# Kernel optimization log

Measured on AMD Instinct MI355X. Metric: run time of the kernel, lower is better.

The kernel has to match this reference:

```python
import jax, jax.numpy as jnp
import numpy as np

N_NODES = 100000
N_EDGES = 1600000
IN_FEATS = 64
N_CLASSES = 64


def setup_inputs() -> dict:
    key = jax.random.key(0)
    k1, k2, k3, k4, k5 = jax.random.split(key, 5)
    feat = jax.random.normal(k1, (N_NODES, IN_FEATS), dtype=jnp.float32)
    edge_row = jnp.sort(jax.random.randint(k2, (N_EDGES,), 0, N_NODES))
    edge_col = jax.random.randint(k3, (N_EDGES,), 0, N_NODES)
    # values of the cached normalized adjacency power (all positive, ~1/deg scale)
    edge_val = jax.random.uniform(k4, (N_EDGES,), dtype=jnp.float32) / 16.0
    # nn.Linear(in_feats, n_classes): weight [C, F] (xavier), bias zeros
    limit = float(np.sqrt(6.0 / (IN_FEATS + N_CLASSES)))
    W = jax.random.uniform(k5, (N_CLASSES, IN_FEATS), dtype=jnp.float32,
                           minval=-limit, maxval=limit)
    b = jnp.zeros((N_CLASSES,), dtype=jnp.float32)
    return {"feat": feat, "edge_row": edge_row, "edge_col": edge_col,
            "edge_val": edge_val, "W": W, "b": b}


def reference(feat, edge_row, edge_col, edge_val, W, b):
    # SpMM: h = A_pre @ feat, A_pre given as COO (edge_row, edge_col, edge_val)
    msg = edge_val[:, None] * feat[edge_col]          # [E, F] gather + scale
    h = jax.ops.segment_sum(msg, edge_row, num_segments=N_NODES)  # [N, F]
    # fc: Linear(in_feats -> n_classes), norm=None so no normalization
    return h @ W.T + b                                 # [N, C]
```

## Files before the change

kernel.cpp:

```cpp
#include <hip/hip_runtime.h>
#include <hip/hip_bf16.h>

typedef __attribute__((ext_vector_type(8))) short short8;
typedef __attribute__((ext_vector_type(4))) float f32x4;

__device__ __forceinline__ unsigned short f2bf(float x) {
    unsigned int u = __float_as_uint(x);
    unsigned int lsb = (u >> 16) & 1u;
    u += 0x7fffu + lsb;
    return (unsigned short)(u >> 16);
}

__device__ __forceinline__ short8 pack8(f32x4 a, f32x4 b) {
    short8 r;
    r[0] = (short)f2bf(a.x); r[1] = (short)f2bf(a.y);
    r[2] = (short)f2bf(a.z); r[3] = (short)f2bf(a.w);
    r[4] = (short)f2bf(b.x); r[5] = (short)f2bf(b.y);
    r[6] = (short)f2bf(b.z); r[7] = (short)f2bf(b.w);
    return r;
}

__global__ __launch_bounds__(256) void k_init(const float* __restrict__ bias,
                                              float* __restrict__ out, long total4) {
    long i4 = (long)blockIdx.x * 256 + threadIdx.x;
    if (i4 < total4) {
        const f32x4* b4 = (const f32x4*)bias;
        ((f32x4*)out)[i4] = b4[i4 & 15];
    }
}

__global__ __launch_bounds__(256) void k_setup(const float* __restrict__ feat,
                                               const float* __restrict__ W,
                                               const float* __restrict__ bias,
                                               unsigned short* __restrict__ G,
                                               float* __restrict__ out,
                                               int N, int gblocks) {
    if ((int)blockIdx.x >= gblocks) {
        long i4 = (long)(blockIdx.x - gblocks) * 256 + threadIdx.x;
        long total4 = (long)N * 16;
        if (i4 < total4) {
            const f32x4* b4 = (const f32x4*)bias;
            ((f32x4*)out)[i4] = b4[i4 & 15];
        }
        return;
    }

    int wave = blockIdx.x * 4 + (threadIdx.x >> 6);
    int lane = threadIdx.x & 63;
    int m0 = wave * 16;
    if (m0 >= N) return;
    int n = lane & 15;
    int quad = lane >> 4;

    short8 bf[4][2];
#pragma unroll
    for (int ct = 0; ct < 4; ++ct)
#pragma unroll
        for (int ks = 0; ks < 2; ++ks) {
            const f32x4* wp = (const f32x4*)(W + (size_t)(ct * 16 + n) * 64 + ks * 32 + quad * 8);
            f32x4 w0 = wp[0];
            f32x4 w1 = wp[1];
            bf[ct][ks] = pack8(w0, w1);
        }

    int mrow = m0 + n; if (mrow >= N) mrow = N - 1;
    short8 af[2];
#pragma unroll
    for (int ks = 0; ks < 2; ++ks) {
        const f32x4* ap = (const f32x4*)(feat + (size_t)mrow * 64 + ks * 32 + quad * 8);
        f32x4 a0 = __builtin_nontemporal_load(ap);
        f32x4 a1 = __builtin_nontemporal_load(ap + 1);
        af[ks] = pack8(a0, a1);
    }

    f32x4 acc[4];
#pragma unroll
    for (int ct = 0; ct < 4; ++ct) {
        acc[ct] = (f32x4){0.f, 0.f, 0.f, 0.f};
#pragma unroll
        for (int ks = 0; ks < 2; ++ks)
            acc[ct] = __builtin_amdgcn_mfma_f32_16x16x32_bf16(af[ks], bf[ct][ks], acc[ct], 0, 0, 0);
    }

#pragma unroll
    for (int ct = 0; ct < 4; ++ct)
#pragma unroll
        for (int r = 0; r < 4; ++r) {
            int rowm = m0 + quad * 4 + r;
            if (rowm < N)
                G[(size_t)rowm * 64 + ct * 16 + n] = f2bf(acc[ct][r]);
        }
}

__global__ __launch_bounds__(256) void k_spmm(const unsigned short* __restrict__ G,
                                              const int* __restrict__ erow,
                                              const int* __restrict__ ecol,
                                              const float* __restrict__ evalv,
                                              const float* __restrict__ bias,
                                              float* __restrict__ out, int E) {
    int b = blockIdx.x;
    int fg  = (b & 7) >> 2;
    int sub = (b >> 3) * 4 + (b & 3);
    int wavein = threadIdx.x >> 6;
    int lane = threadIdx.x & 63;
    long base0 = ((long)sub * 4 + wavein) * 256;
    if (base0 >= E) return;

    int q  = lane >> 4;
    int fs = lane & 15;
    int vq4 = q << 2;
    unsigned voff = (unsigned)fs * 4u;
    const char* Gb = (const char*)G + ((unsigned)fg << 6);
    float2 b2 = ((const float2*)bias)[fg * 16 + fs];

    float acc0 = 0.f, acc1 = 0.f;
    bool first = true;
    int cur;

    auto flush_atomic = [&]() {
        float t0 = acc0 + __shfl_xor(acc0, 16);
        float t1 = acc1 + __shfl_xor(acc1, 16);
        t0 += __shfl_xor(t0, 32);
        t1 += __shfl_xor(t1, 32);
        if (lane < 16) {
            float* p = out + ((size_t)(unsigned)cur << 6) + (unsigned)(fg * 32 + fs * 2);
            atomicAdd(p, t0);
            atomicAdd(p + 1, t1);
        }
        acc0 = 0.f; acc1 = 0.f;
    };
    auto flush = [&]() {
        if (first) { flush_atomic(); first = false; return; }
        float t0 = acc0 + __shfl_xor(acc0, 16);
        float t1 = acc1 + __shfl_xor(acc1, 16);
        t0 += __shfl_xor(t0, 32);
        t1 += __shfl_xor(t1, 32);
        if (lane < 16) {
            float* p = out + ((size_t)(unsigned)cur << 6) + (unsigned)(fg * 32 + fs * 2);
            float2 o; o.x = b2.x + t0; o.y = b2.y + t1;
            *(float2*)p = o;
        }
        acc0 = 0.f; acc1 = 0.f;
    };

    if (base0 + 256 <= E) {
        long i0 = base0 + lane;
        int rv[4], cv[4], vvv[4];
#pragma unroll
        for (int c = 0; c < 4; ++c) {
            rv[c]  = __builtin_nontemporal_load(erow + i0 + 64 * c);
            cv[c]  = __builtin_nontemporal_load(ecol + i0 + 64 * c);
            vvv[c] = __builtin_nontemporal_load((const int*)evalv + i0 + 64 * c);
        }
        cur = __builtin_amdgcn_readlane(rv[0], 0);

        unsigned long long bm[4];
#pragma unroll
        for (int c = 0; c < 4; ++c) {
            int rn = __shfl_down(rv[c], 1);
            unsigned long long m = __ballot(rv[c] != rn) & 0x7fffffffffffffffULL;
            int r63 = __builtin_amdgcn_readlane(rv[c], 63);
            int n0  = (c < 3) ? __builtin_amdgcn_readlane(rv[c + 1], 0) : (r63 + 1);
            if (r63 != n0) m |= 0x8000000000000000ULL;
            bm[c] = m;
        }

        unsigned gbuf[3][8];

#define SPMM_ISSUE(GI, SLOT) do {                                              \
    _Pragma("unroll")                                                          \
    for (int k_ = 0; k_ < 8; ++k_) {                                           \
        const int p_  = (GI) * 8 + k_;                   \
        const int c_  = p_ >> 4;                                    \
        const int pj_ = p_ & 15;                        \
        int idx_ = vq4 + 16 * pj_;                                             \
        int colv_ = __builtin_amdgcn_ds_bpermute(idx_, cv[c_]);                \
        unsigned off_ = ((unsigned)colv_ << 7) + voff;                         \
        gbuf[SLOT][k_] = *(const unsigned*)(Gb + off_);                        \
    } } while (0)

        SPMM_ISSUE(0, 0);
        SPMM_ISSUE(1, 1);

#pragma unroll
        for (int g = 0; g < 8; ++g) {
            if (g < 6) SPMM_ISSUE(g + 2, (g + 2) % 3);
            __builtin_amdgcn_sched_barrier(0);

#pragma unroll
            for (int k = 0; k < 8; ++k) {
                const int p  = g * 8 + k;
                const int c  = p >> 4;
                const int pj = p & 15;
                const int i4 = pj * 4;
                int idx = vq4 + i4 * 4;
                float vs = __int_as_float(__builtin_amdgcn_ds_bpermute(idx, vvv[c]));
                unsigned u = gbuf[g % 3][k];
                float flo = __uint_as_float(u << 16);
                float fhi = __uint_as_float(u & 0xffff0000u);
                bool slow = (pj == 0) ? ((c > 0 && ((bm[c - 1] >> 63) & 1ULL)) || (bm[c] & 7ULL) != 0)
                                      : (((bm[c] >> (4 * pj - 1)) & 0xFULL) != 0);
                if (!slow) {
                    acc0 = fmaf(vs, flo, acc0);
                    acc1 = fmaf(vs, fhi, acc1);
                } else {
                    int r0 = __builtin_amdgcn_readlane(rv[c], i4);
                    int r3 = __builtin_amdgcn_readlane(rv[c], i4 + 3);
                    if (r0 == r3) {
                        if (r0 != cur) { flush(); cur = r0; }
                        acc0 = fmaf(vs, flo, acc0);
                        acc1 = fmaf(vs, fhi, acc1);
                    } else {
                        int rowsv = __builtin_amdgcn_ds_bpermute(idx, rv[c]);
                        int r1 = __builtin_amdgcn_readlane(rv[c], i4 + 1);
                        int r2 = __builtin_amdgcn_readlane(rv[c], i4 + 2);
                        int rr = r0;
                        while (true) {
                            if (rr != cur) { flush(); cur = rr; }
                            float vm = (rowsv == rr) ? vs : 0.f;
                            acc0 = fmaf(vm, flo, acc0);
                            acc1 = fmaf(vm, fhi, acc1);
                            if (rr == r3) break;
                            rr = (r1 > rr) ? r1 : ((r2 > rr) ? r2 : r3);
                        }
                    }
                }
            }
        }
#undef SPMM_ISSUE
    } else {
        cur = erow[base0];
        for (long e = base0; e < (long)E; ++e) {
            int r = erow[e];
            int c = ecol[e];
            float v = evalv[e];
            unsigned u = *(const unsigned*)(Gb + (((unsigned)c << 7) + voff));
            float flo = __uint_as_float(u << 16);
            float fhi = __uint_as_float(u & 0xffff0000u);
            if (r != cur) { flush(); cur = r; }
            float vm = (q == 0) ? v : 0.f;
            acc0 = fmaf(vm, flo, acc0);
            acc1 = fmaf(vm, fhi, acc1);
        }
    }

    flush_atomic();
}

__global__ __launch_bounds__(256) void k_fused(const float* __restrict__ feat,
                                               const int* __restrict__ erow,
                                               const int* __restrict__ ecol,
                                               const float* __restrict__ evalv,
                                               const float* __restrict__ W,
                                               float* __restrict__ out,
                                               int E, int epw) {
    __shared__ float Wt[64 * 64];
    for (int i = threadIdx.x; i < 4096; i += 256) {
        int c = i >> 6, f = i & 63;
        Wt[f * 64 + c] = W[i];
    }
    __syncthreads();

    int wave = blockIdx.x * 4 + (threadIdx.x >> 6);
    int lane = threadIdx.x & 63;
    long e0 = (long)wave * epw;
    if (e0 >= E) return;
    long e1 = e0 + epw; if (e1 > E) e1 = E;

    int cur = erow[e0];
    float acc = 0.f;
    for (long e = e0; e < e1; ++e) {
        int r = erow[e];
        int c = ecol[e];
        float v = evalv[e];
        float g = feat[((size_t)c << 6) | lane];
        if (r != cur) {
            float res = 0.f;
#pragma unroll
            for (int f = 0; f < 64; ++f)
                res += __shfl(acc, f, 64) * Wt[f * 64 + lane];
            atomicAdd(out + ((size_t)cur << 6) + lane, res);
            acc = 0.f;
            cur = r;
        }
        acc += v * g;
    }
    {
        float res = 0.f;
#pragma unroll
        for (int f = 0; f < 64; ++f)
            res += __shfl(acc, f, 64) * Wt[f * 64 + lane];
        atomicAdd(out + ((size_t)cur << 6) + lane, res);
    }
}

extern "C" void kernel_launch(void* const* d_in, const int* in_sizes, int n_in,
                              void* d_out, int out_size, void* d_ws, size_t ws_size,
                              hipStream_t stream) {
    const float* feat  = (const float*)d_in[0];
    const int*   erow  = (const int*)d_in[1];
    const int*   ecol  = (const int*)d_in[2];
    const float* evalv = (const float*)d_in[3];
    const float* W     = (const float*)d_in[4];
    const float* bias  = (const float*)d_in[5];
    float* out = (float*)d_out;

    int N = in_sizes[0] / 64;
    int E = in_sizes[1];

    size_t need = (size_t)N * 64 * sizeof(unsigned short);
    if (ws_size >= need) {
        unsigned short* G = (unsigned short*)d_ws;
        int tiles = (N + 15) / 16;
        int gblocks = (tiles + 3) / 4;
        long total4 = (long)N * 16;
        int iblocks = (int)((total4 + 255) / 256);
        k_setup<<<gblocks + iblocks, 256, 0, stream>>>(feat, W, bias, G, out, N, gblocks);

        int nwpf = (E + 255) / 256;
        int bpf  = (nwpf + 3) / 4;
        int noct = (bpf + 3) / 4;
        k_spmm<<<noct * 8, 256, 0, stream>>>(G, erow, ecol, evalv, bias, out, E);
    } else {
        long total4 = (long)N * 16;
        k_init<<<(int)((total4 + 255) / 256), 256, 0, stream>>>(bias, out, total4);
        int epw = (E + 8191) / 8192;
        if (epw < 32) epw = 32;
        int nwaves = (E + epw - 1) / epw;
        int nblocks = (nwaves + 3) / 4;
        k_fused<<<nblocks, 256, 0, stream>>>(feat, erow, ecol, evalv, W, out, E, epw);
    }
}
```

Before: 164.8 us.

## Quantize projected features to int8 with per-row scales and drop feature-half split

The setup kernel now stores the projected feature matrix as int8 with one float scale per row instead of bf16. The SpMM kernel folds each row's scale into the edge value, and each lane now handles four features instead of two, so one wave covers all 64 features. This removes the two-way feature-group split and halves the bytes gathered per edge. The cost is an extra scattered scale load per edge, heavier dequantization arithmetic, and a notable loss of accuracy from int8 quantization that may break tolerance.

```diff
diff --git a/kernel.cpp b/kernel.cpp
--- a/kernel.cpp
+++ b/kernel.cpp
@@ -32,7 +32,8 @@
 __global__ __launch_bounds__(256) void k_setup(const float* __restrict__ feat,
                                                const float* __restrict__ W,
                                                const float* __restrict__ bias,
-                                               unsigned short* __restrict__ G,
+                                               unsigned char* __restrict__ G8,
+                                               float* __restrict__ scales,
                                                float* __restrict__ out,
                                                int N, int gblocks) {
     if ((int)blockIdx.x >= gblocks) {
@@ -83,64 +84,79 @@
     }
 
 #pragma unroll
-    for (int ct = 0; ct < 4; ++ct)
-#pragma unroll
-        for (int r = 0; r < 4; ++r) {
-            int rowm = m0 + quad * 4 + r;
-            if (rowm < N)
-                G[(size_t)rowm * 64 + ct * 16 + n] = f2bf(acc[ct][r]);
-        }
-}
-
-__global__ __launch_bounds__(256) void k_spmm(const unsigned short* __restrict__ G,
+    for (int r = 0; r < 4; ++r) {
+        float rm = fmaxf(fmaxf(fabsf(acc[0][r]), fabsf(acc[1][r])),
+                         fmaxf(fabsf(acc[2][r]), fabsf(acc[3][r])));
+        rm = fmaxf(rm, __shfl_xor(rm, 1, 16));
+        rm = fmaxf(rm, __shfl_xor(rm, 2, 16));
+        rm = fmaxf(rm, __shfl_xor(rm, 4, 16));
+        rm = fmaxf(rm, __shfl_xor(rm, 8, 16));
+        int rowm = m0 + quad * 4 + r;
+        if (rowm < N) {
+            float inv = (rm > 0.f) ? (127.f / rm) : 0.f;
+            if (n == 0) scales[rowm] = rm * (1.f / 127.f);
+#pragma unroll
+            for (int ct = 0; ct < 4; ++ct) {
+                float qf = rintf(acc[ct][r] * inv);
+                qf = fminf(127.f, fmaxf(-127.f, qf));
+                G8[(size_t)rowm * 64 + ct * 16 + n] = (unsigned char)(signed char)(int)qf;
+            }
+        }
+    }
+}
+
+__global__ __launch_bounds__(256) void k_spmm(const unsigned char* __restrict__ G8,
+                                              const float* __restrict__ scales,
                                               const int* __restrict__ erow,
                                               const int* __restrict__ ecol,
                                               const float* __restrict__ evalv,
                                               const float* __restrict__ bias,
                                               float* __restrict__ out, int E) {
-    int b = blockIdx.x;
-    int fg  = (b & 7) >> 2;
-    int sub = (b >> 3) * 4 + (b & 3);
-    int wavein = threadIdx.x >> 6;
+    int wave = blockIdx.x * 4 + (threadIdx.x >> 6);
     int lane = threadIdx.x & 63;
-    long base0 = ((long)sub * 4 + wavein) * 256;
+    long base0 = (long)wave * 256;
     if (base0 >= E) return;
 
     int q  = lane >> 4;
     int fs = lane & 15;
     int vq4 = q << 2;
     unsigned voff = (unsigned)fs * 4u;
-    const char* Gb = (const char*)G + ((unsigned)fg << 6);
-    float2 b2 = ((const float2*)bias)[fg * 16 + fs];
-
-    float acc0 = 0.f, acc1 = 0.f;
+    f32x4 b4 = ((const f32x4*)bias)[fs];
+
+    float acc0 = 0.f, acc1 = 0.f, acc2 = 0.f, acc3 = 0.f;
     bool first = true;
     int cur;
 
     auto flush_atomic = [&]() {
         float t0 = acc0 + __shfl_xor(acc0, 16);
         float t1 = acc1 + __shfl_xor(acc1, 16);
-        t0 += __shfl_xor(t0, 32);
-        t1 += __shfl_xor(t1, 32);
+        float t2 = acc2 + __shfl_xor(acc2, 16);
+        float t3 = acc3 + __shfl_xor(acc3, 16);
+        t0 += __shfl_xor(t0, 32); t1 += __shfl_xor(t1, 32);
+        t2 += __shfl_xor(t2, 32); t3 += __shfl_xor(t3, 32);
         if (lane < 16) {
-            float* p = out + ((size_t)(unsigned)cur << 6) + (unsigned)(fg * 32 + fs * 2);
-            atomicAdd(p, t0);
+            float* p = out + ((size_t)(unsigned)cur << 6) + ((unsigned)fs << 2);
+            atomicAdd(p + 0, t0);
             atomicAdd(p + 1, t1);
-        }
-        acc0 = 0.f; acc1 = 0.f;
+            atomicAdd(p + 2, t2);
+            atomicAdd(p + 3, t3);
+        }
+        acc0 = acc1 = acc2 = acc3 = 0.f;
     };
     auto flush = [&]() {
         if (first) { flush_atomic(); first = false; return; }
         float t0 = acc0 + __shfl_xor(acc0, 16);
         float t1 = acc1 + __shfl_xor(acc1, 16);
-        t0 += __shfl_xor(t0, 32);
-        t1 += __shfl_xor(t1, 32);
+        float t2 = acc2 + __shfl_xor(acc2, 16);
+        float t3 = acc3 + __shfl_xor(acc3, 16);
+        t0 += __shfl_xor(t0, 32); t1 += __shfl_xor(t1, 32);
+        t2 += __shfl_xor(t2, 32); t3 += __shfl_xor(t3, 32);
         if (lane < 16) {
-            float* p = out + ((size_t)(unsigned)cur << 6) + (unsigned)(fg * 32 + fs * 2);
-            float2 o; o.x = b2.x + t0; o.y = b2.y + t1;
-            *(float2*)p = o;
-        }
-        acc0 = 0.f; acc1 = 0.f;
+            float* p = out + ((size_t)(unsigned)cur << 6) + ((unsigned)fs << 2);
+            f32x4 o = {b4.x + t0, b4.y + t1, b4.z + t2, b4.w + t3};
+            *(f32x4*)p = o;
+        }
+        acc0 = acc1 = acc2 = acc3 = 0.f;
     };
 
     if (base0 + 256 <= E) {
@@ -151,6 +167,8 @@
             rv[c]  = __builtin_nontemporal_load(erow + i0 + 64 * c);
             cv[c]  = __builtin_nontemporal_load(ecol + i0 + 64 * c);
             vvv[c] = __builtin_nontemporal_load((const int*)evalv + i0 + 64 * c);
+            float sc = scales[(unsigned)cv[c]];
+            vvv[c] = __float_as_int(__int_as_float(vvv[c]) * sc);
         }
         cur = __builtin_amdgcn_readlane(rv[0], 0);
 
@@ -175,8 +193,8 @@
         const int pj_ = p_ & 15;                        \
         int idx_ = vq4 + 16 * pj_;                                             \
         int colv_ = __builtin_amdgcn_ds_bpermute(idx_, cv[c_]);                \
-        unsigned off_ = ((unsigned)colv_ << 7) + voff;                         \
-        gbuf[SLOT][k_] = *(const unsigned*)(Gb + off_);                        \
+        unsigned off_ = ((unsigned)colv_ << 6) + voff;                         \
+        gbuf[SLOT][k_] = *(const unsigned*)(G8 + off_);                        \
     } } while (0)
 
         SPMM_ISSUE(0, 0);
@@ -196,20 +214,26 @@
                 int idx = vq4 + i4 * 4;
                 float vs = __int_as_float(__builtin_amdgcn_ds_bpermute(idx, vvv[c]));
                 unsigned u = gbuf[g % 3][k];
-                float flo = __uint_as_float(u << 16);
-                float fhi = __uint_as_float(u & 0xffff0000u);
+                float f0 = (float)((int)(u << 24) >> 24);
+                float f1 = (float)((int)(u << 16) >> 24);
+                float f2 = (float)((int)(u << 8) >> 24);
+                float f3 = (float)((int)u >> 24);
                 bool slow = (pj == 0) ? ((c > 0 && ((bm[c - 1] >> 63) & 1ULL)) || (bm[c] & 7ULL) != 0)
                                       : (((bm[c] >> (4 * pj - 1)) & 0xFULL) != 0);
                 if (!slow) {
-                    acc0 = fmaf(vs, flo, acc0);
-                    acc1 = fmaf(vs, fhi, acc1);
+                    acc0 = fmaf(vs, f0, acc0);
+                    acc1 = fmaf(vs, f1, acc1);
+                    acc2 = fmaf(vs, f2, acc2);
+                    acc3 = fmaf(vs, f3, acc3);
                 } else {
                     int r0 = __builtin_amdgcn_readlane(rv[c], i4);
                     int r3 = __builtin_amdgcn_readlane(rv[c], i4 + 3);
                     if (r0 == r3) {
                         if (r0 != cur) { flush(); cur = r0; }
-                        acc0 = fmaf(vs, flo, acc0);
-                        acc1 = fmaf(vs, fhi, acc1);
+                        acc0 = fmaf(vs, f0, acc0);
+                        acc1 = fmaf(vs, f1, acc1);
+                        acc2 = fmaf(vs, f2, acc2);
+                        acc3 = fmaf(vs, f3, acc3);
                     } else {
                         int rowsv = __builtin_amdgcn_ds_bpermute(idx, rv[c]);
                         int r1 = __builtin_amdgcn_readlane(rv[c], i4 + 1);
@@ -218,8 +242,10 @@
                         while (true) {
                             if (rr != cur) { flush(); cur = rr; }
                             float vm = (rowsv == rr) ? vs : 0.f;
-                            acc0 = fmaf(vm, flo, acc0);
-                            acc1 = fmaf(vm, fhi, acc1);
+                            acc0 = fmaf(vm, f0, acc0);
+                            acc1 = fmaf(vm, f1, acc1);
+                            acc2 = fmaf(vm, f2, acc2);
+                            acc3 = fmaf(vm, f3, acc3);
                             if (rr == r3) break;
                             rr = (r1 > rr) ? r1 : ((r2 > rr) ? r2 : r3);
                         }
@@ -233,14 +259,18 @@
         for (long e = base0; e < (long)E; ++e) {
             int r = erow[e];
             int c = ecol[e];
-            float v = evalv[e];
-            unsigned u = *(const unsigned*)(Gb + (((unsigned)c << 7) + voff));
-            float flo = __uint_as_float(u << 16);
-            float fhi = __uint_as_float(u & 0xffff0000u);
+            float v = evalv[e] * scales[(unsigned)c];
+            unsigned u = *(const unsigned*)(G8 + (((unsigned)c << 6) + voff));
+            float f0 = (float)((int)(u << 24) >> 24);
+            float f1 = (float)((int)(u << 16) >> 24);
+            float f2 = (float)((int)(u << 8) >> 24);
+            float f3 = (float)((int)u >> 24);
             if (r != cur) { flush(); cur = r; }
             float vm = (q == 0) ? v : 0.f;
-            acc0 = fmaf(vm, flo, acc0);
-            acc1 = fmaf(vm, fhi, acc1);
+            acc0 = fmaf(vm, f0, acc0);
+            acc1 = fmaf(vm, f1, acc1);
+            acc2 = fmaf(vm, f2, acc2);
+            acc3 = fmaf(vm, f3, acc3);
         }
     }
 
@@ -308,19 +338,19 @@
     int N = in_sizes[0] / 64;
     int E = in_sizes[1];
 
-    size_t need = (size_t)N * 64 * sizeof(unsigned short);
+    size_t need = (size_t)N * 64 + (size_t)N * 4;
     if (ws_size >= need) {
-        unsigned short* G = (unsigned short*)d_ws;
+        unsigned char* G8 = (unsigned char*)d_ws;
+        float* scales = (float*)((char*)d_ws + (size_t)N * 64);
         int tiles = (N + 15) / 16;
         int gblocks = (tiles + 3) / 4;
         long total4 = (long)N * 16;
         int iblocks = (int)((total4 + 255) / 256);
-        k_setup<<<gblocks + iblocks, 256, 0, stream>>>(feat, W, bias, G, out, N, gblocks);
-
-        int nwpf = (E + 255) / 256;
-        int bpf  = (nwpf + 3) / 4;
-        int noct = (bpf + 3) / 4;
-        k_spmm<<<noct * 8, 256, 0, stream>>>(G, erow, ecol, evalv, bias, out, E);
+        k_setup<<<gblocks + iblocks, 256, 0, stream>>>(feat, W, bias, G8, scales, out, N, gblocks);
+
+        int nwaves = (E + 255) / 256;
+        int nblocks = (nwaves + 3) / 4;
+        k_spmm<<<nblocks, 256, 0, stream>>>(G8, scales, erow, ecol, evalv, bias, out, E);
     } else {
         long total4 = (long)N * 16;
         k_init<<<(int)((total4 + 255) / 256), 256, 0, stream>>>(bias, out, total4);
```

Result: faster. 158.8 us (-3.6%).
